# Kernel tuning notes

Hardware: AMD Instinct MI355X
Metric: run time of the kernel (lower is better)

The kernel has to match this reference:

```python
import jax, jax.numpy as jnp
import numpy as np

B, L, D_MODEL, D_STATE, D_HIDDEN = 4, 4096, 1024, 256, 4096
RMIN, RMAX, MAX_PHASE = 0.8, 0.95, 2.0 * np.pi


def setup_inputs() -> dict:
    key = jax.random.key(0)
    ks = jax.random.split(key, 10)
    # LRU ring init (Orvieto et al.): |lambda| in [rmin, rmax], phase in [0, max_phase)
    u1 = jax.random.uniform(ks[0], (D_STATE,))
    u2 = jax.random.uniform(ks[1], (D_STATE,))
    nu_log = jnp.log(-0.5 * jnp.log(u1 * (RMAX**2 - RMIN**2) + RMIN**2))
    theta_log = jnp.log(MAX_PHASE * u2)
    B_re = jax.random.normal(ks[2], (D_STATE, D_MODEL)) / np.sqrt(2.0 * D_MODEL)
    B_im = jax.random.normal(ks[3], (D_STATE, D_MODEL)) / np.sqrt(2.0 * D_MODEL)
    C_re = jax.random.normal(ks[4], (D_MODEL, D_STATE)) / np.sqrt(D_STATE)
    C_im = jax.random.normal(ks[5], (D_MODEL, D_STATE)) / np.sqrt(D_STATE)
    D_mat = jax.random.normal(ks[6], (D_MODEL, D_MODEL)) / np.sqrt(D_MODEL)
    W1 = jax.random.normal(ks[7], (D_MODEL, D_HIDDEN)) * np.sqrt(2.0 / D_MODEL)
    W2 = jax.random.normal(ks[8], (D_HIDDEN, D_MODEL)) * np.sqrt(2.0 / D_HIDDEN)
    res_logit = jnp.asarray(-1.0, dtype=jnp.float32)
    x3d = jax.random.normal(ks[9], (B, L, D_MODEL), dtype=jnp.float32)
    return {"x3d": x3d, "nu_log": nu_log, "theta_log": theta_log,
            "B_re": B_re, "B_im": B_im, "C_re": C_re, "C_im": C_im,
            "D_mat": D_mat, "W1": W1, "W2": W2, "res_logit": res_logit}


def _lru_scan(lam, Bu):
    # diagonal linear recurrence x_t = lam * x_{t-1} + Bu_t via associative scan
    lam_b = jnp.broadcast_to(lam, Bu.shape)  # [B, L, N]

    def comb(a, b):
        return (a[0] * b[0], b[0] * a[1] + b[1])

    _, states = jax.lax.associative_scan(comb, (lam_b, Bu), axis=1)
    return states  # [B, L, N] complex


def reference(x3d, nu_log, theta_log, B_re, B_im, C_re, C_im, D_mat, W1, W2, res_logit):
    lam = jnp.exp(-jnp.exp(nu_log) + 1j * jnp.exp(theta_log))          # [N]
    gamma = jnp.sqrt(1.0 - jnp.abs(lam) ** 2)                           # [N]
    Bn = (gamma[:, None] * (B_re + 1j * B_im))                          # [N, D]
    Bu = jnp.einsum('bld,nd->bln', x3d.astype(jnp.complex64), Bn)       # [B, L, N]
    states = _lru_scan(lam.astype(jnp.complex64), Bu)                   # [B, L, N]
    y = jnp.einsum('bln,mn->blm', states, C_re + 1j * C_im).real \
        + jnp.einsum('bld,md->blm', x3d, D_mat)                         # [B, L, D]
    # MLP feedforward (nl_layers=2, bias=False), dropout is identity at p=0
    z = jax.nn.gelu(y @ W1) @ W2                                        # [B, L, D]
    out = x3d + jax.nn.sigmoid(res_logit) * z
    st = states[:, -1]  # final recurrent state
    return out, st
```

## Files before the change

kernel.cpp:

```cpp
#include <hip/hip_runtime.h>
#include <stdint.h>

typedef __bf16 bf16;
typedef bf16 bf16x8 __attribute__((ext_vector_type(8)));
typedef float f32x4 __attribute__((ext_vector_type(4)));

#define B_  4
#define L_  4096
#define DM  1024
#define DS  256
#define DH  4096
#define BL  16384
#define CL  64
#define NC  64

__device__ __forceinline__ float bfbits(uint32_t lo16) {
  union { uint32_t u; float f; } v; v.u = lo16 << 16; return v.f;
}

__device__ __forceinline__ void async16(const bf16* g, bf16* l) {
  __builtin_amdgcn_global_load_lds(
      (const __attribute__((address_space(1))) uint32_t*)g,
      (__attribute__((address_space(3))) uint32_t*)l, 16, 0, 0);
}

__global__ void phaseA(const float* __restrict__ nu_log,
                       const float* __restrict__ th_log,
                       float* __restrict__ scal) {
  int n = threadIdx.x;
  float nu = __expf(nu_log[n]);
  float th = __expf(th_log[n]);
  float mod = __expf(-nu);
  float lr = mod * cosf(th);
  float li = mod * sinf(th);
  float g = sqrtf(fmaxf(1.0f - mod * mod, 0.0f));
  float pr = 1.f, pi = 0.f;
  for (int i = 0; i < CL; i++) {
    float nr = pr * lr - pi * li;
    float ni = pr * li + pi * lr;
    pr = nr; pi = ni;
  }
  scal[n] = lr; scal[256 + n] = li;
  scal[512 + n] = pr; scal[768 + n] = pi;
  scal[1024 + n] = g;
}

__global__ void prep_bu(const float* __restrict__ B_re, const float* __restrict__ B_im,
                        const float* __restrict__ scal, bf16* __restrict__ WB) {
  size_t i = (size_t)blockIdx.x * 256 + threadIdx.x;
  int row = (int)(i >> 10), col = (int)(i & 1023);
  int n = row >> 1;
  const float* src = (row & 1) ? B_im : B_re;
  WB[i] = (bf16)(scal[1024 + n] * src[n * 1024 + col]);
}

__global__ void prep_y(const float* __restrict__ C_re, const float* __restrict__ C_im,
                       const float* __restrict__ D_mat, bf16* __restrict__ WB) {
  size_t i = (size_t)blockIdx.x * 256 + threadIdx.x;
  int m = (int)(i / 1536), c = (int)(i % 1536);
  float v;
  if (c < 256)       v = C_re[m * 256 + c];
  else if (c < 512)  v = -C_im[m * 256 + (c - 256)];
  else               v = D_mat[m * 1024 + (c - 512)];
  WB[i] = (bf16)v;
}

__global__ void transpose_to_bf16(const float* __restrict__ in, bf16* __restrict__ out,
                                  int R, int C) {
  __shared__ float tile[32][33];
  int c0 = blockIdx.x * 32, r0 = blockIdx.y * 32;
  int tx = threadIdx.x, ty = threadIdx.y;
  for (int i = 0; i < 32; i += 8)
    tile[ty + i][tx] = in[(size_t)(r0 + ty + i) * C + c0 + tx];
  __syncthreads();
  for (int i = 0; i < 32; i += 8)
    out[(size_t)(c0 + ty + i) * R + r0 + tx] = (bf16)tile[tx][ty + i];
}

__global__ void conv_x(const float4* __restrict__ x, bf16* __restrict__ XS) {
  size_t i = (size_t)blockIdx.x * 256 + threadIdx.x;
  size_t t = i >> 8;
  int d4 = (int)(i & 255);
  float4 v = x[i];
  bf16* o = XS + t * 1536 + 512 + (size_t)d4 * 4;
  o[0] = (bf16)v.x; o[1] = (bf16)v.y; o[2] = (bf16)v.z; o[3] = (bf16)v.w;
}

template <int EPI>
__global__ __launch_bounds__(256, 3) void gemm_bt(
    const bf16* __restrict__ A, int lda,
    const bf16* __restrict__ Bt, int ldb,
    void* __restrict__ C, int ldc, int K, int mt, int nt,
    const float* __restrict__ xres, const float* __restrict__ reslog) {
  __shared__ __align__(16) bf16 sAb[3 * 128 * 32];
  __shared__ __align__(16) bf16 sBb[3 * 128 * 32];
  int tid = threadIdx.x;
  int wave = tid >> 6, lane = tid & 63;
  int q = lane >> 4, l16 = lane & 15;
  int wm = (wave & 1) * 64, wn = (wave >> 1) * 64;

  int nb = mt * nt;
  int per = nb >> 3;
  int t = (blockIdx.x & 7) * per + (blockIdx.x >> 3);
  int gsz = 8 * nt;
  int g = t / gsz, r = t % gsz;
  int tm = g * 8 + (r & 7);
  int tn = r >> 3;
  size_t m0 = (size_t)tm * 128, n0 = (size_t)tn * 128;

  f32x4 acc[4][4] = {};

  int stg_fe[2];
  const bf16* gpA[2];
  const bf16* gpB[2];
#pragma unroll
  for (int cc = 0; cc < 2; cc++) {
    int chunk = wave * 2 + cc;
    int fe = (chunk * 64 + lane) * 8;
    stg_fe[cc] = fe;
    gpA[cc] = A + (m0 + (fe >> 5)) * (size_t)lda + (fe & 31);
    gpB[cc] = Bt + (n0 + (fe >> 5)) * (size_t)ldb + (fe & 31);
  }

  int NI = K >> 5;
#pragma unroll
  for (int b = 0; b < 2; b++)
#pragma unroll
    for (int cc = 0; cc < 2; cc++) {
      async16(gpA[cc] + b * 32, &sAb[b * 4096 + stg_fe[cc]]);
      async16(gpB[cc] + b * 32, &sBb[b * 4096 + stg_fe[cc]]);
    }

  int p = 0, p2 = 2;
  for (int i = 0; i < NI; i++) {
    if (i + 1 < NI) __builtin_amdgcn_s_waitcnt(0x0F74);
    else            __builtin_amdgcn_s_waitcnt(0x0F70);
    __builtin_amdgcn_s_barrier();
    asm volatile("" ::: "memory");

    const bf16* a_base = &sAb[p * 4096];
    const bf16* b_base = &sBb[p * 4096];
    bf16x8 afr[4], bfr[4];
#pragma unroll
    for (int i4 = 0; i4 < 4; i4++)
      afr[i4] = *(const bf16x8*)&a_base[(wm + i4 * 16 + l16) * 32 + q * 8];
#pragma unroll
    for (int i4 = 0; i4 < 4; i4++)
      bfr[i4] = *(const bf16x8*)&b_base[(wn + i4 * 16 + l16) * 32 + q * 8];

    if (i + 2 < NI) {
      int k2 = (i + 2) * 32;
#pragma unroll
      for (int cc = 0; cc < 2; cc++) {
        async16(gpA[cc] + k2, &sAb[p2 * 4096 + stg_fe[cc]]);
        async16(gpB[cc] + k2, &sBb[p2 * 4096 + stg_fe[cc]]);
      }
    }

#pragma unroll
    for (int mi = 0; mi < 4; mi++)
#pragma unroll
      for (int ni = 0; ni < 4; ni++)
        acc[mi][ni] = __builtin_amdgcn_mfma_f32_16x16x32_bf16(afr[mi], bfr[ni], acc[mi][ni], 0, 0, 0);

    p = (p == 2) ? 0 : p + 1;
    p2 = (p2 == 2) ? 0 : p2 + 1;
  }

  float sig = 0.f;
  if (EPI == 2) sig = 1.f / (1.f + __expf(-reslog[0]));
#pragma unroll
  for (int mi = 0; mi < 4; mi++)
#pragma unroll
    for (int ni = 0; ni < 4; ni++) {
      size_t col = n0 + wn + ni * 16 + l16;
#pragma unroll
      for (int r2 = 0; r2 < 4; r2++) {
        size_t row = m0 + wm + mi * 16 + q * 4 + r2;
        float v = acc[mi][ni][r2];
        size_t off = row * (size_t)ldc + col;
        if (EPI == 0) {
          ((bf16*)C)[off] = (bf16)v;
        } else if (EPI == 1) {
          float z = 0.7978845608f * (v + 0.044715f * v * v * v);
          float gv = v / (1.f + __expf(-2.f * z));
          ((bf16*)C)[off] = (bf16)gv;
        } else {
          ((float*)C)[off] = xres[off] + sig * v;
        }
      }
    }
}

__global__ void scan_pass1(const bf16* __restrict__ Bu, const float* __restrict__ scal,
                           float2* __restrict__ H) {
  int b = blockIdx.x >> 6, c = blockIdx.x & 63, n = threadIdx.x;
  float lr = scal[n], li = scal[256 + n];
  float sr = 0.f, si = 0.f;
  size_t t0 = (size_t)b * L_ + (size_t)c * CL;
  const uint32_t* p = (const uint32_t*)(Bu + t0 * 512) + n;
  for (int j = 0; j < CL; j++) {
    uint32_t u = p[(size_t)j * 256];
    float ur = bfbits(u & 0xffffu), ui = bfbits(u >> 16);
    float nr = lr * sr - li * si + ur;
    float ni = lr * si + li * sr + ui;
    sr = nr; si = ni;
  }
  H[(size_t)(b * NC + c) * 256 + n] = make_float2(sr, si);
}

__global__ void scan_pass2(const float2* __restrict__ H, const float* __restrict__ scal,
                           float2* __restrict__ Carry) {
  int b = blockIdx.x, n = threadIdx.x;
  float Pr = scal[512 + n], Pi = scal[768 + n];
  float cr = 0.f, ci = 0.f;
  for (int c = 0; c < NC; c++) {
    Carry[(size_t)(b * NC + c) * 256 + n] = make_float2(cr, ci);
    float2 h = H[(size_t)(b * NC + c) * 256 + n];
    float nr = Pr * cr - Pi * ci + h.x;
    float ni = Pr * ci + Pi * cr + h.y;
    cr = nr; ci = ni;
  }
}

__global__ void scan_pass3(const bf16* __restrict__ Bu, const float* __restrict__ scal,
                           const float2* __restrict__ Carry, bf16* __restrict__ XS,
                           float* __restrict__ st) {
  int b = blockIdx.x >> 6, c = blockIdx.x & 63, n = threadIdx.x;
  float lr = scal[n], li = scal[256 + n];
  float2 cv = Carry[(size_t)(b * NC + c) * 256 + n];
  float sr = cv.x, si = cv.y;
  size_t t0 = (size_t)b * L_ + (size_t)c * CL;
  const uint32_t* p = (const uint32_t*)(Bu + t0 * 512) + n;
  bf16* qp = XS + t0 * 1536 + n;
  for (int j = 0; j < CL; j++) {
    uint32_t u = p[(size_t)j * 256];
    float ur = bfbits(u & 0xffffu), ui = bfbits(u >> 16);
    float nr = lr * sr - li * si + ur;
    float ni = lr * si + li * sr + ui;
    sr = nr; si = ni;
    qp[(size_t)j * 1536] = (bf16)sr;
    qp[(size_t)j * 1536 + 256] = (bf16)si;
  }
  if (c == NC - 1) {
    st[(size_t)b * 256 + n] = sr;
    st[1024 + (size_t)b * 256 + n] = si;
  }
}

extern "C" void kernel_launch(void* const* d_in, const int* in_sizes, int n_in,
                              void* d_out, int out_size, void* d_ws, size_t ws_size,
                              hipStream_t stream) {
  const float* x      = (const float*)d_in[0];
  const float* nu_log = (const float*)d_in[1];
  const float* th_log = (const float*)d_in[2];
  const float* B_re   = (const float*)d_in[3];
  const float* B_im   = (const float*)d_in[4];
  const float* C_re   = (const float*)d_in[5];
  const float* C_im   = (const float*)d_in[6];
  const float* D_mat  = (const float*)d_in[7];
  const float* W1     = (const float*)d_in[8];
  const float* W2     = (const float*)d_in[9];
  const float* reslog = (const float*)d_in[10];

  char* wsb = (char*)d_ws;
  size_t off = 0;
  auto alloc = [&](size_t bytes) {
    void* p = wsb + off;
    off += (bytes + 255) & ~(size_t)255;
    return p;
  };
  float*  scal = (float*)alloc(5 * 256 * 4);
  bf16*   WBbu = (bf16*)alloc((size_t)512 * 1024 * 2);
  bf16*   WBy  = (bf16*)alloc((size_t)1024 * 1536 * 2);
  bf16*   WB1  = (bf16*)alloc((size_t)4096 * 1024 * 2);
  bf16*   WB2  = (bf16*)alloc((size_t)1024 * 4096 * 2);
  float2* H    = (float2*)alloc((size_t)B_ * NC * 256 * 8);
  float2* Cr   = (float2*)alloc((size_t)B_ * NC * 256 * 8);
  bf16*   Ybf  = (bf16*)alloc((size_t)BL * 1024 * 2);
  bf16*   XS   = (bf16*)alloc((size_t)BL * 1536 * 2);
  bf16*   Bu   = (bf16*)alloc((size_t)BL * 512 * 2);
  bf16*   Hbf  = XS;

  float* out = (float*)d_out;
  float* st  = out + (size_t)BL * DM;

  phaseA<<<1, 256, 0, stream>>>(nu_log, th_log, scal);
  prep_bu<<<512 * 1024 / 256, 256, 0, stream>>>(B_re, B_im, scal, WBbu);
  prep_y<<<1024 * 1536 / 256, 256, 0, stream>>>(C_re, C_im, D_mat, WBy);
  transpose_to_bf16<<<dim3(4096 / 32, 1024 / 32), dim3(32, 8), 0, stream>>>(W1, WB1, 1024, 4096);
  transpose_to_bf16<<<dim3(1024 / 32, 4096 / 32), dim3(32, 8), 0, stream>>>(W2, WB2, 4096, 1024);
  conv_x<<<BL * 256 / 256, 256, 0, stream>>>((const float4*)x, XS);

  gemm_bt<0><<<128 * 4, 256, 0, stream>>>(
      XS + 512, 1536, WBbu, 1024, Bu, 512, 1024, 128, 4, nullptr, nullptr);

  scan_pass1<<<B_ * NC, 256, 0, stream>>>(Bu, scal, H);
  scan_pass2<<<B_, 256, 0, stream>>>(H, scal, Cr);
  scan_pass3<<<B_ * NC, 256, 0, stream>>>(Bu, scal, Cr, XS, st);

  gemm_bt<0><<<128 * 8, 256, 0, stream>>>(
      XS, 1536, WBy, 1536, Ybf, 1024, 1536, 128, 8, nullptr, nullptr);

  for (int i = 0; i < 2; i++) {
    const bf16* Yc = Ybf + (size_t)i * 8192 * 1024;
    float* Oc = out + (size_t)i * 8192 * 1024;
    const float* Xc = x + (size_t)i * 8192 * 1024;
    gemm_bt<1><<<64 * 32, 256, 0, stream>>>(
        Yc, 1024, WB1, 1024, Hbf, 4096, 1024, 64, 32, nullptr, nullptr);
    gemm_bt<2><<<64 * 8, 256, 0, stream>>>(
        Hbf, 4096, WB2, 4096, Oc, 1024, 4096, 64, 8, Xc, reslog);
  }
}
```

Before: 638.6 us.

## Replace 128x128 GEMM with 256x256-tile 8-wave ping-pong pipelined kernel

Replaces the 128x128-tile, 4-wave GEMM with a 256x256-tile, 512-thread kernel that uses BK=64, double-buffered LDS with an XOR swizzle, and an interleaved staging/MFMA schedule using barriers and s_setprio. Each wave computes a 128x64 sub-tile in four quadrant phases, and global-to-LDS loads for the next k-steps are issued between the phases. The aim is more operand reuse per byte loaded and better overlap of loads with MFMA. In exchange, far fewer blocks are launched (e.g. 128 blocks for the first GEMM, 128 for the W2 GEMM), which risks leaving CUs idle on a 256-CU part, and accumulator register pressure rises.

```diff
diff --git a/kernel.cpp b/kernel.cpp
--- a/kernel.cpp
+++ b/kernel.cpp
@@ -86,97 +86,154 @@
   o[0] = (bf16)v.x; o[1] = (bf16)v.y; o[2] = (bf16)v.z; o[3] = (bf16)v.w;
 }
 
+#define SYNC_PRE()  do { asm volatile("" ::: "memory"); __builtin_amdgcn_s_barrier(); } while (0)
+#define SYNC_POST() do { __builtin_amdgcn_s_barrier(); asm volatile("" ::: "memory"); } while (0)
+
 template <int EPI>
-__global__ __launch_bounds__(256, 3) void gemm_bt(
+__global__ __launch_bounds__(512, 2) void gemm256(
     const bf16* __restrict__ A, int lda,
     const bf16* __restrict__ Bt, int ldb,
-    void* __restrict__ C, int ldc, int K, int mt, int nt,
+    void* __restrict__ C, int ldc, int NK, int mt, int nt,
     const float* __restrict__ xres, const float* __restrict__ reslog) {
-  __shared__ __align__(16) bf16 sAb[3 * 128 * 32];
-  __shared__ __align__(16) bf16 sBb[3 * 128 * 32];
-  int tid = threadIdx.x;
-  int wave = tid >> 6, lane = tid & 63;
-  int q = lane >> 4, l16 = lane & 15;
-  int wm = (wave & 1) * 64, wn = (wave >> 1) * 64;
+  __shared__ __align__(16) bf16 sA[2 * 2 * 8192];
+  __shared__ __align__(16) bf16 sB[2 * 2 * 8192];
+
+  const int tid  = threadIdx.x;
+  const int lane = tid & 63;
+  const int wave = tid >> 6;
+  const int q = lane >> 4, l16 = lane & 15;
+  const int wr = wave >> 2, wc = wave & 3;
 
   int nb = mt * nt;
   int per = nb >> 3;
-  int t = (blockIdx.x & 7) * per + (blockIdx.x >> 3);
-  int gsz = 8 * nt;
-  int g = t / gsz, r = t % gsz;
-  int tm = g * 8 + (r & 7);
-  int tn = r >> 3;
-  size_t m0 = (size_t)tm * 128, n0 = (size_t)tn * 128;
-
-  f32x4 acc[4][4] = {};
-
-  int stg_fe[2];
-  const bf16* gpA[2];
-  const bf16* gpB[2];
-#pragma unroll
-  for (int cc = 0; cc < 2; cc++) {
-    int chunk = wave * 2 + cc;
-    int fe = (chunk * 64 + lane) * 8;
-    stg_fe[cc] = fe;
-    gpA[cc] = A + (m0 + (fe >> 5)) * (size_t)lda + (fe & 31);
-    gpB[cc] = Bt + (n0 + (fe >> 5)) * (size_t)ldb + (fe & 31);
-  }
-
-  int NI = K >> 5;
-#pragma unroll
-  for (int b = 0; b < 2; b++)
-#pragma unroll
-    for (int cc = 0; cc < 2; cc++) {
-      async16(gpA[cc] + b * 32, &sAb[b * 4096 + stg_fe[cc]]);
-      async16(gpB[cc] + b * 32, &sBb[b * 4096 + stg_fe[cc]]);
+  int t0 = (blockIdx.x & 7) * per + (blockIdx.x >> 3);
+  int gsz = nt << 3;
+  int g = t0 / gsz, r = t0 % gsz;
+  size_t m0 = (size_t)(g * 8 + (r & 7)) * 256;
+  size_t n0 = (size_t)(r >> 3) * 256;
+
+  const int srow = tid >> 3;
+  const int scol = ((tid & 7) << 3) ^ ((srow & 12) << 2);
+  const bf16* gA = A  + (m0 + srow) * (size_t)lda + scol;
+  const bf16* gB = Bt + (n0 + srow) * (size_t)ldb + scol;
+  bf16* lA = sA + tid * 8;
+  bf16* lB = sB + tid * 8;
+
+  auto stageA = [&](int kt, int w) {
+    const bf16* s = gA + (size_t)(w * 128) * lda + kt * 64;
+    bf16* l = lA + ((kt & 1) * 16384 + w * 8192);
+    async16(s, l);
+    async16(s + (size_t)64 * lda, l + 4096);
+  };
+  auto stageB = [&](int kt, int w) {
+    const bf16* s = gB + (size_t)(w * 128) * ldb + kt * 64;
+    bf16* l = lB + ((kt & 1) * 16384 + w * 8192);
+    async16(s, l);
+    async16(s + (size_t)64 * ldb, l + 4096);
+  };
+
+  stageB(0, 0); stageB(0, 1); stageA(0, 0); stageA(0, 1);
+  stageB(1, 0); stageB(1, 1); stageA(1, 0);
+  __builtin_amdgcn_s_waitcnt(0x0F76);
+  __builtin_amdgcn_s_barrier();
+  asm volatile("" ::: "memory");
+
+  const int sw  = (l16 & 12) << 2;
+  const int qx0 = (q << 3) ^ sw;
+  const int qx1 = ((q << 3) + 32) ^ sw;
+  const bf16* Ard = sA + wr * 8192 + l16 * 64;
+  const bf16* Brd = sB + (wc >> 1) * 8192 + ((wc & 1) * 64 + l16) * 64;
+
+  f32x4 acc[8][4] = {};
+  bf16x8 a[4][2], b[4][2];
+
+  for (int t = 0; t < NK; ++t) {
+    const int d = (t & 1) * 16384;
+    const bf16* Ab = Ard + d;
+    const bf16* Bb = Brd + d;
+
+#pragma unroll
+    for (int j = 0; j < 4; ++j) {
+      a[j][0] = *(const bf16x8*)&Ab[j * 1024 + qx0];
+      a[j][1] = *(const bf16x8*)&Ab[j * 1024 + qx1];
     }
-
-  int p = 0, p2 = 2;
-  for (int i = 0; i < NI; i++) {
-    if (i + 1 < NI) __builtin_amdgcn_s_waitcnt(0x0F74);
-    else            __builtin_amdgcn_s_waitcnt(0x0F70);
-    __builtin_amdgcn_s_barrier();
-    asm volatile("" ::: "memory");
-
-    const bf16* a_base = &sAb[p * 4096];
-    const bf16* b_base = &sBb[p * 4096];
-    bf16x8 afr[4], bfr[4];
-#pragma unroll
-    for (int i4 = 0; i4 < 4; i4++)
-      afr[i4] = *(const bf16x8*)&a_base[(wm + i4 * 16 + l16) * 32 + q * 8];
-#pragma unroll
-    for (int i4 = 0; i4 < 4; i4++)
-      bfr[i4] = *(const bf16x8*)&b_base[(wn + i4 * 16 + l16) * 32 + q * 8];
-
-    if (i + 2 < NI) {
-      int k2 = (i + 2) * 32;
-#pragma unroll
-      for (int cc = 0; cc < 2; cc++) {
-        async16(gpA[cc] + k2, &sAb[p2 * 4096 + stg_fe[cc]]);
-        async16(gpB[cc] + k2, &sBb[p2 * 4096 + stg_fe[cc]]);
-      }
+#pragma unroll
+    for (int n = 0; n < 4; ++n) {
+      b[n][0] = *(const bf16x8*)&Bb[n * 1024 + qx0];
+      b[n][1] = *(const bf16x8*)&Bb[n * 1024 + qx1];
     }
-
-#pragma unroll
-    for (int mi = 0; mi < 4; mi++)
-#pragma unroll
-      for (int ni = 0; ni < 4; ni++)
-        acc[mi][ni] = __builtin_amdgcn_mfma_f32_16x16x32_bf16(afr[mi], bfr[ni], acc[mi][ni], 0, 0, 0);
-
-    p = (p == 2) ? 0 : p + 1;
-    p2 = (p2 == 2) ? 0 : p2 + 1;
+    if (t + 1 < NK) stageA(t + 1, 1);
+    SYNC_PRE();
+    asm volatile("s_waitcnt lgkmcnt(0)" ::: "memory");
+    __builtin_amdgcn_s_setprio(1);
+#pragma unroll
+    for (int j = 0; j < 4; ++j)
+#pragma unroll
+      for (int n = 0; n < 2; ++n) {
+        acc[j][n] = __builtin_amdgcn_mfma_f32_16x16x32_bf16(a[j][0], b[n][0], acc[j][n], 0, 0, 0);
+        acc[j][n] = __builtin_amdgcn_mfma_f32_16x16x32_bf16(a[j][1], b[n][1], acc[j][n], 0, 0, 0);
+      }
+    __builtin_amdgcn_s_setprio(0);
+    SYNC_POST();
+
+    if (t + 2 < NK) stageB(t + 2, 0);
+    SYNC_PRE();
+    __builtin_amdgcn_s_setprio(1);
+#pragma unroll
+    for (int j = 0; j < 4; ++j)
+#pragma unroll
+      for (int n = 0; n < 2; ++n) {
+        acc[j][2 + n] = __builtin_amdgcn_mfma_f32_16x16x32_bf16(a[j][0], b[2 + n][0], acc[j][2 + n], 0, 0, 0);
+        acc[j][2 + n] = __builtin_amdgcn_mfma_f32_16x16x32_bf16(a[j][1], b[2 + n][1], acc[j][2 + n], 0, 0, 0);
+      }
+    __builtin_amdgcn_s_setprio(0);
+    SYNC_POST();
+
+#pragma unroll
+    for (int j = 0; j < 4; ++j) {
+      a[j][0] = *(const bf16x8*)&Ab[(4 + j) * 1024 + qx0];
+      a[j][1] = *(const bf16x8*)&Ab[(4 + j) * 1024 + qx1];
+    }
+    if (t + 2 < NK) stageB(t + 2, 1);
+    SYNC_PRE();
+    asm volatile("s_waitcnt lgkmcnt(0)" ::: "memory");
+    __builtin_amdgcn_s_setprio(1);
+#pragma unroll
+    for (int j = 0; j < 4; ++j)
+#pragma unroll
+      for (int n = 0; n < 2; ++n) {
+        acc[4 + j][n] = __builtin_amdgcn_mfma_f32_16x16x32_bf16(a[j][0], b[n][0], acc[4 + j][n], 0, 0, 0);
+        acc[4 + j][n] = __builtin_amdgcn_mfma_f32_16x16x32_bf16(a[j][1], b[n][1], acc[4 + j][n], 0, 0, 0);
+      }
+    __builtin_amdgcn_s_setprio(0);
+    SYNC_POST();
+
+    if (t + 2 < NK) stageA(t + 2, 0);
+    if (t + 2 < NK)      __builtin_amdgcn_s_waitcnt(0x0F76);
+    else if (t + 1 < NK) __builtin_amdgcn_s_waitcnt(0x0F70);
+    SYNC_PRE();
+    __builtin_amdgcn_s_setprio(1);
+#pragma unroll
+    for (int j = 0; j < 4; ++j)
+#pragma unroll
+      for (int n = 0; n < 2; ++n) {
+        acc[4 + j][2 + n] = __builtin_amdgcn_mfma_f32_16x16x32_bf16(a[j][0], b[2 + n][0], acc[4 + j][2 + n], 0, 0, 0);
+        acc[4 + j][2 + n] = __builtin_amdgcn_mfma_f32_16x16x32_bf16(a[j][1], b[2 + n][1], acc[4 + j][2 + n], 0, 0, 0);
+      }
+    __builtin_amdgcn_s_setprio(0);
+    SYNC_POST();
   }
 
   float sig = 0.f;
   if (EPI == 2) sig = 1.f / (1.f + __expf(-reslog[0]));
 #pragma unroll
-  for (int mi = 0; mi < 4; mi++)
-#pragma unroll
-    for (int ni = 0; ni < 4; ni++) {
-      size_t col = n0 + wn + ni * 16 + l16;
-#pragma unroll
-      for (int r2 = 0; r2 < 4; r2++) {
-        size_t row = m0 + wm + mi * 16 + q * 4 + r2;
+  for (int mi = 0; mi < 8; ++mi)
+#pragma unroll
+    for (int ni = 0; ni < 4; ++ni) {
+      size_t col = n0 + wc * 64 + ni * 16 + l16;
+#pragma unroll
+      for (int r2 = 0; r2 < 4; ++r2) {
+        size_t row = m0 + wr * 128 + mi * 16 + q * 4 + r2;
         float v = acc[mi][ni][r2];
         size_t off = row * (size_t)ldc + col;
         if (EPI == 0) {
@@ -292,23 +349,23 @@
   transpose_to_bf16<<<dim3(1024 / 32, 4096 / 32), dim3(32, 8), 0, stream>>>(W2, WB2, 4096, 1024);
   conv_x<<<BL * 256 / 256, 256, 0, stream>>>((const float4*)x, XS);
 
-  gemm_bt<0><<<128 * 4, 256, 0, stream>>>(
-      XS + 512, 1536, WBbu, 1024, Bu, 512, 1024, 128, 4, nullptr, nullptr);
+  gemm256<0><<<64 * 2, 512, 0, stream>>>(
+      XS + 512, 1536, WBbu, 1024, Bu, 512, 16, 64, 2, nullptr, nullptr);
 
   scan_pass1<<<B_ * NC, 256, 0, stream>>>(Bu, scal, H);
   scan_pass2<<<B_, 256, 0, stream>>>(H, scal, Cr);
   scan_pass3<<<B_ * NC, 256, 0, stream>>>(Bu, scal, Cr, XS, st);
 
-  gemm_bt<0><<<128 * 8, 256, 0, stream>>>(
-      XS, 1536, WBy, 1536, Ybf, 1024, 1536, 128, 8, nullptr, nullptr);
+  gemm256<0><<<64 * 4, 512, 0, stream>>>(
+      XS, 1536, WBy, 1536, Ybf, 1024, 24, 64, 4, nullptr, nullptr);
 
   for (int i = 0; i < 2; i++) {
     const bf16* Yc = Ybf + (size_t)i * 8192 * 1024;
     float* Oc = out + (size_t)i * 8192 * 1024;
     const float* Xc = x + (size_t)i * 8192 * 1024;
-    gemm_bt<1><<<64 * 32, 256, 0, stream>>>(
-        Yc, 1024, WB1, 1024, Hbf, 4096, 1024, 64, 32, nullptr, nullptr);
-    gemm_bt<2><<<64 * 8, 256, 0, stream>>>(
-        Hbf, 4096, WB2, 4096, Oc, 1024, 4096, 64, 8, Xc, reslog);
-  }
-}
+    gemm256<1><<<32 * 16, 512, 0, stream>>>(
+        Yc, 1024, WB1, 1024, Hbf, 4096, 16, 32, 16, nullptr, nullptr);
+    gemm256<2><<<32 * 4, 512, 0, stream>>>(
+        Hbf, 4096, WB2, 4096, Oc, 1024, 64, 32, 4, Xc, reslog);
+  }
+}
```

Result: slower. 723.0 us (+13.2%).
